# Performance work log

Measured on AMD Instinct MI355X. Metric: run time of the kernel, lower is better.

## Reference

```python
import jax, jax.numpy as jnp
import numpy as np

B, S, D = 8, 1024, 256
H = 8            # num_heads
HD = D // H      # head_dim
FF = 1024        # expert hidden_dim
E = 8            # num_experts
K = 2            # top-k
L = 2            # num_layers
OUT = 1000       # output_dim
EPS = 1e-5


def setup_inputs() -> dict:
    key = jax.random.key(0)
    ks = jax.random.split(key, 20)
    std = 0.02
    inp = {
        "x": jax.random.normal(ks[0], (B, S, D), jnp.float32),
        "qkv_w": jax.random.normal(ks[1], (L, D, 3 * D), jnp.float32) * std,
        "qkv_b": jnp.zeros((L, 3 * D), jnp.float32),
        "attn_w": jax.random.normal(ks[2], (L, D, D), jnp.float32) * std,
        "attn_b": jnp.zeros((L, D), jnp.float32),
        "gate_w": jax.random.normal(ks[3], (L, D, E), jnp.float32) * std,
        "gate_b": jnp.zeros((L, E), jnp.float32),
        "e_w1": jax.random.normal(ks[4], (L, E, D, FF), jnp.float32) * std,
        "e_b1": jnp.zeros((L, E, FF), jnp.float32),
        "e_w2": jax.random.normal(ks[5], (L, E, FF, D), jnp.float32) * std,
        "e_b2": jnp.zeros((L, E, D), jnp.float32),
        "ln1_g": jnp.ones((D,), jnp.float32),
        "ln1_b": jnp.zeros((D,), jnp.float32),
        "ln2_g": jnp.ones((D,), jnp.float32),
        "ln2_b": jnp.zeros((D,), jnp.float32),
        "head_w": jax.random.normal(ks[6], (D, OUT), jnp.float32) * std,
        "head_b": jnp.zeros((OUT,), jnp.float32),
    }
    return inp


def _layer_norm(x, g, b):
    m = jnp.mean(x, -1, keepdims=True)
    v = jnp.mean((x - m) ** 2, -1, keepdims=True)
    return (x - m) / jnp.sqrt(v + EPS) * g + b


def _attention(x, w_qkv, b_qkv, w_o, b_o):
    # x: [B,S,D]
    qkv = (x @ w_qkv + b_qkv).reshape(B, S, 3, H, HD)
    q, k, v = jnp.moveaxis(qkv, 2, 0)            # each [B,S,H,HD]
    q = q.transpose(0, 2, 1, 3)                   # [B,H,S,HD]
    k = k.transpose(0, 2, 1, 3)
    v = v.transpose(0, 2, 1, 3)
    attn = jax.nn.softmax(jnp.einsum('bhqd,bhkd->bhqk', q, k) * (HD ** -0.5), axis=-1)
    o = jnp.einsum('bhqk,bhkd->bhqd', attn, v).transpose(0, 2, 1, 3).reshape(B, S, D)
    return o @ w_o + b_o


def _moe(x, gw, gb, w1, b1, w2, b2):
    # x: [B,S,D] -> tokens [T,D]
    xf = x.reshape(-1, D)
    gates = xf @ gw + gb                           # [T,E]
    scores, idx = jax.lax.top_k(gates, K)          # [T,K]
    gate_w = jax.nn.softmax(scores, axis=-1)       # [T,K]
    # dense all-expert compute, then gather selected experts per token
    h = jax.nn.gelu(jnp.einsum('td,edh->teh', xf, w1) + b1, approximate=False)
    eo = jnp.einsum('teh,ehd->ted', h, w2) + b2    # [T,E,D]
    sel = jnp.take_along_axis(eo, idx[:, :, None], axis=1)  # [T,K,D]
    out = jnp.sum(gate_w[:, :, None] * sel, axis=1)
    return out.reshape(B, S, D)


def reference(x, qkv_w, qkv_b, attn_w, attn_b, gate_w, gate_b,
              e_w1, e_b1, e_w2, e_b2, ln1_g, ln1_b, ln2_g, ln2_b,
              head_w, head_b):
    for l in range(L):
        x = x + _attention(_layer_norm(x, ln1_g, ln1_b),
                           qkv_w[l], qkv_b[l], attn_w[l], attn_b[l])
        x = x + _moe(_layer_norm(x, ln2_g, ln2_b),
                     gate_w[l], gate_b[l], e_w1[l], e_b1[l], e_w2[l], e_b2[l])
    pooled = jnp.mean(x, axis=1)                   # [B,D]
    return pooled @ head_w + head_b                # [B,OUT]
```

## Files before the change

### kernel.cpp

```cpp
#include <hip/hip_runtime.h>
#include <math.h>

#define TOK   8192
#define DIM   256
#define NH    8
#define HDIM  32
#define FFD   1024
#define NE    8
#define NL    2
#define NOUT  1000
#define NSLOT 16384

typedef unsigned int uint;
typedef unsigned short ushort;
typedef __attribute__((ext_vector_type(8))) short short8;
typedef __attribute__((ext_vector_type(4))) float f32x4;

#define WS_X     ((size_t)0)
#define WS_LN    (WS_X    + (size_t)TOK*DIM)
#define WS_QKV   (WS_LN   + (size_t)TOK*DIM)
#define WS_H     (WS_QKV  + (size_t)TOK*3*DIM)
#define WS_SOUT  (WS_H    + (size_t)NSLOT*256)
#define WS_GV    (WS_SOUT + (size_t)NSLOT*256)
#define WS_PP    (WS_GV   + (size_t)TOK*2)
#define WS_POOL  (WS_PP   + (size_t)8*32*256)
#define WS_INT   (WS_POOL + (size_t)8*256)
#define WS_U16   (WS_INT  + (size_t)54144)
#define WS_BIG   (WS_U16  + (size_t)2359296)

#define IB_COUNTS   0
#define IB_NTILES   8
#define IB_OFFS     16
#define IB_CURS     24
#define IB_TILE_E   32
#define IB_TILE_R0  320
#define IB_TILE_RE  608
#define IB_GIDX     896
#define IB_SPOS     17280
#define IB_STOK     33664
#define IB_BLKC     50048
#define IB_BLKB     52096

__device__ __forceinline__ float gelu_exact(float v) {
    return 0.5f * v * (1.0f + erff(v * 0.70710678118654752f));
}

__device__ __forceinline__ ushort rnd_bf16(float x) {
    uint u = __float_as_uint(x);
    return (ushort)((u + 0x7FFFu + ((u >> 16) & 1u)) >> 16);
}

__device__ __forceinline__ float bf16_f32(ushort h) {
    return __uint_as_float(((uint)h) << 16);
}

__device__ __forceinline__ void split2(float x, ushort& h, ushort& lo) {
    uint u = __float_as_uint(x);
    uint hh = (u + 0x7FFFu + ((u >> 16) & 1u)) >> 16;
    h = (ushort)hh;
    float hf = __uint_as_float(hh << 16);
    float l = x - hf;
    uint ul = __float_as_uint(l);
    lo = (ushort)((ul + 0x7FFFu + ((ul >> 16) & 1u)) >> 16);
}

__device__ __forceinline__ void gld16(const ushort* g, ushort* l) {
    __builtin_amdgcn_global_load_lds(
        (const __attribute__((address_space(1))) uint*)g,
        (__attribute__((address_space(3))) uint*)l, 16, 0, 0);
}

template<bool WF32>
__global__ __launch_bounds__(256) void ln_split(const float* __restrict__ x,
                                                float* __restrict__ out,
                                                ushort* __restrict__ ohi,
                                                const float* __restrict__ g,
                                                const float* __restrict__ b) {
    int wave = threadIdx.x >> 6;
    int lane = threadIdx.x & 63;
    int t = blockIdx.x * 4 + wave;
    const float* xp = x + (size_t)t * DIM;
    float4 v = *(const float4*)&xp[lane * 4];
    float s = v.x + v.y + v.z + v.w;
    #pragma unroll
    for (int off = 32; off; off >>= 1) s += __shfl_xor(s, off);
    float mean = s * (1.0f / 256.0f);
    float dx = v.x - mean, dy = v.y - mean, dz = v.z - mean, dw = v.w - mean;
    float vs = dx * dx + dy * dy + dz * dz + dw * dw;
    #pragma unroll
    for (int off = 32; off; off >>= 1) vs += __shfl_xor(vs, off);
    float inv = rsqrtf(vs * (1.0f / 256.0f) + 1e-5f);
    float4 gg = *(const float4*)&g[lane * 4];
    float4 bb = *(const float4*)&b[lane * 4];
    float o0 = dx * inv * gg.x + bb.x;
    float o1 = dy * inv * gg.y + bb.y;
    float o2 = dz * inv * gg.z + bb.z;
    float o3 = dw * inv * gg.w + bb.w;
    size_t idx = (size_t)t * DIM + lane * 4;
    if (WF32) {
        float4 o; o.x = o0; o.y = o1; o.z = o2; o.w = o3;
        *(float4*)&out[idx] = o;
    }
    uint2 ph;
    ph.x = (uint)rnd_bf16(o0) | ((uint)rnd_bf16(o1) << 16);
    ph.y = (uint)rnd_bf16(o2) | ((uint)rnd_bf16(o3) << 16);
    *(uint2*)&ohi[idx] = ph;
}

template<bool WLO>
__global__ __launch_bounds__(256) void split_transpose(const float* __restrict__ src,
                                                       ushort* __restrict__ dhi,
                                                       ushort* __restrict__ dlo,
                                                       int K, int N) {
    int z = blockIdx.z;
    const float* s = src + (size_t)z * K * N;
    ushort* th = dhi + (size_t)z * K * N;
    ushort* tl = dlo + (size_t)z * K * N;
    __shared__ float tile[32][33];
    int k0 = blockIdx.x * 32, n0 = blockIdx.y * 32;
    int tx = threadIdx.x & 31, ty = threadIdx.x >> 5;
    #pragma unroll
    for (int i = 0; i < 4; ++i) {
        int k = k0 + ty + i * 8;
        tile[ty + i * 8][tx] = s[(size_t)k * N + n0 + tx];
    }
    __syncthreads();
    #pragma unroll
    for (int i = 0; i < 4; ++i) {
        int n = n0 + ty + i * 8;
        float v = tile[tx][ty + i * 8];
        ushort h, lo;
        split2(v, h, lo);
        th[(size_t)n * K + k0 + tx] = h;
        if (WLO) tl[(size_t)n * K + k0 + tx] = lo;
    }
}


template<int MODE, int APASS>
__global__ __launch_bounds__(256) void mfma_dense128x64(const ushort* __restrict__ Ah,
                                                        const ushort* __restrict__ Al,
                                                        const ushort* __restrict__ Bh,
                                                        const ushort* __restrict__ Bl,
                                                        const float* __restrict__ bias,
                                                        float* __restrict__ C,
                                                        ushort* __restrict__ Chi, int N) {
    __shared__ ushort LAh[128][32], LBh[64][32], LBl[64][32];
    __shared__ ushort LAl[APASS == 2 ? 128 : 2][32];
    int tid = threadIdx.x;
    int w = tid >> 6, l = tid & 63, c = l & 15, G = l >> 4;
    int row0 = blockIdx.y * 128, col0 = blockIdx.x * 64;
    int lr = l >> 2, sd = l & 3;
    int rA0 = w * 16 + lr, rA1 = 64 + rA0;
    size_t ga0 = (size_t)(row0 + rA0) * 256 + ((sd ^ ((rA0 >> 1) & 3)) << 3);
    size_t ga1 = (size_t)(row0 + rA1) * 256 + ((sd ^ ((rA1 >> 1) & 3)) << 3);
    size_t gb0 = (size_t)(col0 + rA0) * 256 + ((sd ^ ((rA0 >> 1) & 3)) << 3);
    ushort* dA0h = &LAh[w * 16][0];      ushort* dA1h = &LAh[64 + w * 16][0];
    ushort* dBh  = &LBh[w * 16][0];      ushort* dBl  = &LBl[w * 16][0];
    f32x4 acc[2][4] = {};
    for (int k0 = 0; k0 < 256; k0 += 32) {
        gld16(&Ah[ga0 + k0], dA0h);
        gld16(&Ah[ga1 + k0], dA1h);
        if (APASS == 2) {
            gld16(&Al[ga0 + k0], &LAl[w * 16][0]);
            gld16(&Al[ga1 + k0], &LAl[64 + w * 16][0]);
        }
        gld16(&Bh[gb0 + k0], dBh);
        gld16(&Bl[gb0 + k0], dBl);
        __syncthreads();
        int ar = w * 32 + c;
        short8 a_h[2], a_l[2];
        #pragma unroll
        for (int i = 0; i < 2; ++i) {
            int r = ar + i * 16;
            int sg = (G ^ ((r >> 1) & 3)) << 3;
            a_h[i] = *(const short8*)&LAh[r][sg];
            if (APASS == 2) a_l[i] = *(const short8*)&LAl[r][sg];
        }
        #pragma unroll
        for (int j = 0; j < 4; ++j) {
            int r = j * 16 + c;
            int sg = (G ^ ((r >> 1) & 3)) << 3;
            short8 b_h = *(const short8*)&LBh[r][sg];
            short8 b_l = *(const short8*)&LBl[r][sg];
            #pragma unroll
            for (int i = 0; i < 2; ++i) {
                acc[i][j] = __builtin_amdgcn_mfma_f32_16x16x32_bf16(a_h[i], b_h, acc[i][j], 0, 0, 0);
                acc[i][j] = __builtin_amdgcn_mfma_f32_16x16x32_bf16(a_h[i], b_l, acc[i][j], 0, 0, 0);
                if (APASS == 2)
                    acc[i][j] = __builtin_amdgcn_mfma_f32_16x16x32_bf16(a_l[i], b_h, acc[i][j], 0, 0, 0);
            }
        }
        __syncthreads();
    }
    int rbase = row0 + w * 32 + G * 4;
    #pragma unroll
    for (int i = 0; i < 2; ++i) {
        #pragma unroll
        for (int j = 0; j < 4; ++j) {
            int gc = col0 + j * 16 + c;
            float bv = bias[gc];
            #pragma unroll
            for (int rr = 0; rr < 4; ++rr) {
                int grow = rbase + i * 16 + rr;
                size_t idx = (size_t)grow * N + gc;
                float v = acc[i][j][rr] + bv;
                if (MODE == 1) v += C[idx];
                if (MODE == 3) {
                    Chi[idx] = rnd_bf16(v);
                } else {
                    C[idx] = v;
                }
            }
        }
    }
}

__global__ __launch_bounds__(256) void vt_kernel(const ushort* __restrict__ qkvh,
                                                 ushort* __restrict__ vth) {
    int bh = blockIdx.y;
    int b = bh >> 3, h = bh & 7;
    int kv0 = blockIdx.x * 32;
    __shared__ ushort smh[32][33];
    int tid = threadIdx.x;
    #pragma unroll
    for (int p = 0; p < 4; ++p) {
        int kv = p * 8 + (tid >> 5);
        int d = tid & 31;
        size_t src = ((size_t)(b * 1024 + kv0 + kv)) * 768 + 512 + h * 32 + d;
        smh[kv][d] = qkvh[src];
    }
    __syncthreads();
    #pragma unroll
    for (int p = 0; p < 4; ++p) {
        int d = p * 8 + (tid >> 5);
        int kv = tid & 31;
        size_t dst = ((size_t)(bh * 32 + d)) * 1024 + kv0 + kv;
        vth[dst] = smh[kv][d];
    }
}

__global__ __launch_bounds__(256, 4) void attention_mfma(const ushort* __restrict__ qkvh,
                                                         const ushort* __restrict__ vth,
                                                         ushort* __restrict__ ohi) {
    int b = blockIdx.z, h = blockIdx.y;
    int q0 = blockIdx.x * 64;
    int tid = threadIdx.x;
    int w = tid >> 6, l = tid & 63;
    int c = l & 15, g = l >> 4;
    __shared__ ushort Kh[64][40];
    __shared__ ushort VTh[32][72];
    __shared__ ushort Ph[4][16][76];

    size_t qbase = ((size_t)(b * 1024 + q0 + w * 16 + c)) * 768 + h * 32 + g * 8;
    short8 qa_h = *(const short8*)&qkvh[qbase];

    f32x4 acc_o[2] = {};
    float lpart[4] = {0.f, 0.f, 0.f, 0.f};
    const float scale = 0.17677669529663687f;

    int sr = tid >> 2, sc8 = (tid & 3) * 8;
    size_t kgbase = ((size_t)(b * 1024 + sr)) * 768 + 256 + h * 32 + sc8;
    int vd = tid >> 3, vk8 = (tid & 7) * 8;
    size_t vtbase = ((size_t)((b * 8 + h) * 32 + vd)) * 1024 + vk8;

    for (int kv0 = 0; kv0 < 1024; kv0 += 64) {
        __syncthreads();
        *(uint4*)&Kh[sr][sc8]  = *(const uint4*)&qkvh[kgbase + (size_t)kv0 * 768];
        *(uint4*)&VTh[vd][vk8] = *(const uint4*)&vth[vtbase + kv0];
        __syncthreads();

        f32x4 s4[4];
        #pragma unroll
        for (int t = 0; t < 4; ++t) {
            short8 kh = *(const short8*)&Kh[t * 16 + c][g * 8];
            f32x4 a = {};
            a = __builtin_amdgcn_mfma_f32_16x16x32_bf16(qa_h, kh, a, 0, 0, 0);
            s4[t] = a;
        }

        #pragma unroll
        for (int rr = 0; rr < 4; ++rr) {
            float sum = 0.f;
            #pragma unroll
            for (int t = 0; t < 4; ++t) {
                float p = __expf(s4[t][rr] * scale);
                uint u = __float_as_uint(p);
                uint r = (u + 0x7FFFu + ((u >> 16) & 1u)) >> 16;
                Ph[w][g * 4 + rr][t * 16 + c] = (ushort)r;
                sum += __uint_as_float(r << 16);
            }
            lpart[rr] += sum;
        }
        asm volatile("s_waitcnt lgkmcnt(0)" ::: "memory");

        #pragma unroll
        for (int kt = 0; kt < 2; ++kt) {
            short8 pah = *(const short8*)&Ph[w][c][kt * 32 + g * 8];
            #pragma unroll
            for (int T = 0; T < 2; ++T) {
                short8 vh = *(const short8*)&VTh[T * 16 + c][kt * 32 + g * 8];
                acc_o[T] = __builtin_amdgcn_mfma_f32_16x16x32_bf16(pah, vh, acc_o[T], 0, 0, 0);
            }
        }
    }

    #pragma unroll
    for (int rr = 0; rr < 4; ++rr) {
        float s = lpart[rr];
        s += __shfl_xor(s, 1);
        s += __shfl_xor(s, 2);
        s += __shfl_xor(s, 4);
        s += __shfl_xor(s, 8);
        lpart[rr] = s;
    }

    #pragma unroll
    for (int rr = 0; rr < 4; ++rr) {
        float inv = 1.0f / lpart[rr];
        int q = q0 + w * 16 + g * 4 + rr;
        #pragma unroll
        for (int T = 0; T < 2; ++T) {
            float v = acc_o[T][rr] * inv;
            size_t idx = (size_t)(b * 1024 + q) * 256 + h * 32 + T * 16 + c;
            ohi[idx] = rnd_bf16(v);
        }
    }
}

__global__ __launch_bounds__(256) void mfma_ffn1_12864(const ushort* __restrict__ Ah,
                                                       const ushort* __restrict__ W1h,
                                                       const float* __restrict__ b1l,
                                                       ushort* __restrict__ hh,
                                                       const int* __restrict__ ib,
                                                       int c0, int hFF) {
    int tileIdx = blockIdx.y;
    if (tileIdx >= ib[IB_NTILES]) return;
    int e = ib[IB_TILE_E + tileIdx];
    int row0 = ib[IB_TILE_R0 + tileIdx];
    int rowend = ib[IB_TILE_RE + tileIdx];
    __shared__ ushort LAh[128][32], LBh[64][32];
    __shared__ int tok[128];
    int tid = threadIdx.x;
    if (tid < 128) {
        int sr = row0 + tid;
        tok[tid] = ib[IB_STOK + (sr < rowend ? sr : row0)];
    }
    __syncthreads();
    int w = tid >> 6, l = tid & 63, c = l & 15, G = l >> 4;
    int lr = l >> 2, sd = l & 3;
    int rA0 = w * 16 + lr, rA1 = 64 + rA0;
    int colbase = blockIdx.x * 64;
    const ushort* Bh = W1h + (size_t)e * 262144 + (size_t)(c0 + colbase) * 256;
    size_t ga0 = (size_t)tok[rA0] * 256 + ((sd ^ ((rA0 >> 1) & 3)) << 3);
    size_t ga1 = (size_t)tok[rA1] * 256 + ((sd ^ ((rA1 >> 1) & 3)) << 3);
    size_t gb0 = (size_t)rA0 * 256 + ((sd ^ ((rA0 >> 1) & 3)) << 3);
    ushort* dA0h = &LAh[w * 16][0];      ushort* dA1h = &LAh[64 + w * 16][0];
    ushort* dBh  = &LBh[w * 16][0];
    f32x4 acc[2][4] = {};
    for (int k0 = 0; k0 < 256; k0 += 32) {
        gld16(&Ah[ga0 + k0], dA0h);
        gld16(&Ah[ga1 + k0], dA1h);
        gld16(&Bh[gb0 + k0], dBh);
        __syncthreads();
        int ar = w * 32 + c;
        short8 a_h[2];
        #pragma unroll
        for (int i = 0; i < 2; ++i) {
            int r = ar + i * 16;
            int sg = (G ^ ((r >> 1) & 3)) << 3;
            a_h[i] = *(const short8*)&LAh[r][sg];
        }
        #pragma unroll
        for (int j = 0; j < 4; ++j) {
            int r = j * 16 + c;
            int sg = (G ^ ((r >> 1) & 3)) << 3;
            short8 b_h = *(const short8*)&LBh[r][sg];
            #pragma unroll
            for (int i = 0; i < 2; ++i) {
                acc[i][j] = __builtin_amdgcn_mfma_f32_16x16x32_bf16(a_h[i], b_h, acc[i][j], 0, 0, 0);
            }
        }
        __syncthreads();
    }
    int rbase = row0 + w * 32 + G * 4;
    #pragma unroll
    for (int i = 0; i < 2; ++i) {
        #pragma unroll
        for (int j = 0; j < 4; ++j) {
            int cl = colbase + j * 16 + c;
            float bv = b1l[(size_t)e * FFD + c0 + cl];
            #pragma unroll
            for (int rr = 0; rr < 4; ++rr) {
                int sr = rbase + i * 16 + rr;
                if (sr < rowend) {
                    float v = gelu_exact(acc[i][j][rr] + bv);
                    hh[(size_t)sr * hFF + cl] = rnd_bf16(v);
                }
            }
        }
    }
}

template<bool OUT16>
__global__ __launch_bounds__(256) void mfma_ffn2_12864(const ushort* __restrict__ Ah,
                                                       const ushort* __restrict__ W2h,
                                                       const float* __restrict__ b2l,
                                                       float* __restrict__ soutf,
                                                       ushort* __restrict__ soutb,
                                                       const int* __restrict__ ib,
                                                       int c0, int hFF) {
    int tileIdx = blockIdx.y;
    if (tileIdx >= ib[IB_NTILES]) return;
    int e = ib[IB_TILE_E + tileIdx];
    int row0 = ib[IB_TILE_R0 + tileIdx];
    int rowend = ib[IB_TILE_RE + tileIdx];
    __shared__ ushort LAh[128][32], LBh[64][32];
    int tid = threadIdx.x;
    int w = tid >> 6, l = tid & 63, c = l & 15, G = l >> 4;
    int lr = l >> 2, sd = l & 3;
    int rA0 = w * 16 + lr, rA1 = 64 + rA0;
    int colbase = blockIdx.x * 64;
    const ushort* Bh = W2h + (size_t)e * 262144;
    size_t ga0 = (size_t)(row0 + rA0) * hFF + ((sd ^ ((rA0 >> 1) & 3)) << 3);
    size_t ga1 = (size_t)(row0 + rA1) * hFF + ((sd ^ ((rA1 >> 1) & 3)) << 3);
    size_t gb0 = (size_t)(colbase + rA0) * 1024 + c0 + ((sd ^ ((rA0 >> 1) & 3)) << 3);
    ushort* dA0h = &LAh[w * 16][0];      ushort* dA1h = &LAh[64 + w * 16][0];
    ushort* dBh  = &LBh[w * 16][0];
    f32x4 acc[2][4] = {};
    for (int k0 = 0; k0 < hFF; k0 += 32) {
        gld16(&Ah[ga0 + k0], dA0h);
        gld16(&Ah[ga1 + k0], dA1h);
        gld16(&Bh[gb0 + k0], dBh);
        __syncthreads();
        int ar = w * 32 + c;
        short8 a_h[2];
        #pragma unroll
        for (int i = 0; i < 2; ++i) {
            int r = ar + i * 16;
            int sg = (G ^ ((r >> 1) & 3)) << 3;
            a_h[i] = *(const short8*)&LAh[r][sg];
        }
        #pragma unroll
        for (int j = 0; j < 4; ++j) {
            int r = j * 16 + c;
            int sg = (G ^ ((r >> 1) & 3)) << 3;
            short8 b_h = *(const short8*)&LBh[r][sg];
            #pragma unroll
            for (int i = 0; i < 2; ++i) {
                acc[i][j] = __builtin_amdgcn_mfma_f32_16x16x32_bf16(a_h[i], b_h, acc[i][j], 0, 0, 0);
            }
        }
        __syncthreads();
    }
    int rbase = row0 + w * 32 + G * 4;
    #pragma unroll
    for (int i = 0; i < 2; ++i) {
        #pragma unroll
        for (int j = 0; j < 4; ++j) {
            int n = colbase + j * 16 + c;
            float bv = b2l[(size_t)e * DIM + n];
            #pragma unroll
            for (int rr = 0; rr < 4; ++rr) {
                int sr = rbase + i * 16 + rr;
                if (sr < rowend) {
                    size_t idx = (size_t)sr * 256 + n;
                    if (OUT16) {
                        soutb[idx] = rnd_bf16(acc[i][j][rr] + bv);
                    } else {
                        if (c0 == 0) soutf[idx] = acc[i][j][rr] + bv;
                        else         soutf[idx] += acc[i][j][rr];
                    }
                }
            }
        }
    }
}

__global__ __launch_bounds__(256) void gate_topk(const float* __restrict__ lnb,
                                                 const float* __restrict__ gw,
                                                 const float* __restrict__ gb,
                                                 float* __restrict__ gv, int* __restrict__ ib) {
    __shared__ int hist[8];
    int tid = threadIdx.x;
    if (tid < 8) hist[tid] = 0;
    __syncthreads();
    int grp = tid >> 3, ln8 = tid & 7;
    int t = blockIdx.x * 32 + grp;
    const float* x = lnb + (size_t)t * DIM + ln8 * 32;
    const float* wb = gw + (size_t)ln8 * 32 * 8;
    float g[8] = {};
    #pragma unroll
    for (int d4 = 0; d4 < 8; ++d4) {
        float4 xv = *(const float4*)&x[d4 * 4];
        const float* wr = wb + d4 * 32;
        float4 wa0 = *(const float4*)&wr[0],  wb0 = *(const float4*)&wr[4];
        float4 wa1 = *(const float4*)&wr[8],  wb1 = *(const float4*)&wr[12];
        float4 wa2 = *(const float4*)&wr[16], wb2 = *(const float4*)&wr[20];
        float4 wa3 = *(const float4*)&wr[24], wb3 = *(const float4*)&wr[28];
        g[0] += xv.x * wa0.x + xv.y * wa1.x + xv.z * wa2.x + xv.w * wa3.x;
        g[1] += xv.x * wa0.y + xv.y * wa1.y + xv.z * wa2.y + xv.w * wa3.y;
        g[2] += xv.x * wa0.z + xv.y * wa1.z + xv.z * wa2.z + xv.w * wa3.z;
        g[3] += xv.x * wa0.w + xv.y * wa1.w + xv.z * wa2.w + xv.w * wa3.w;
        g[4] += xv.x * wb0.x + xv.y * wb1.x + xv.z * wb2.x + xv.w * wb3.x;
        g[5] += xv.x * wb0.y + xv.y * wb1.y + xv.z * wb2.y + xv.w * wb3.y;
        g[6] += xv.x * wb0.z + xv.y * wb1.z + xv.z * wb2.z + xv.w * wb3.z;
        g[7] += xv.x * wb0.w + xv.y * wb1.w + xv.z * wb2.w + xv.w * wb3.w;
    }
    #pragma unroll
    for (int e = 0; e < 8; ++e) {
        g[e] += __shfl_xor(g[e], 1);
        g[e] += __shfl_xor(g[e], 2);
        g[e] += __shfl_xor(g[e], 4);
    }
    if (ln8 == 0) {
        #pragma unroll
        for (int e = 0; e < 8; ++e) g[e] += gb[e];
        int i0 = 0; float s0 = g[0];
        #pragma unroll
        for (int e = 1; e < 8; ++e) if (g[e] > s0) { s0 = g[e]; i0 = e; }
        int i1 = -1; float s1 = -1e30f;
        #pragma unroll
        for (int e = 0; e < 8; ++e) if (e != i0 && g[e] > s1) { s1 = g[e]; i1 = e; }
        float e1 = __expf(s1 - s0);
        float w0v = 1.0f / (1.0f + e1);
        float w1v = e1 / (1.0f + e1);
        gv[2 * t] = w0v; gv[2 * t + 1] = w1v;
        ib[IB_GIDX + 2 * t] = i0; ib[IB_GIDX + 2 * t + 1] = i1;
        atomicAdd(&hist[i0], 1);
        atomicAdd(&hist[i1], 1);
    }
    __syncthreads();
    if (tid < 8) ib[IB_BLKC + blockIdx.x * 8 + tid] = hist[tid];
}

__global__ __launch_bounds__(256) void scan_tiles(int* ib) {
    __shared__ int bc[2048], bb[2048];
    __shared__ int counts[8], offs[8], tstart[9];
    int tid = threadIdx.x;
    for (int i = tid; i < 2048; i += 256) bc[i] = ib[IB_BLKC + i];
    __syncthreads();
    if (tid < 8) {
        int run = 0;
        for (int b = 0; b < 256; ++b) {
            bb[b * 8 + tid] = run;
            run += bc[b * 8 + tid];
        }
        counts[tid] = run;
    }
    __syncthreads();
    if (tid == 0) {
        int off = 0, ts = 0;
        for (int e = 0; e < 8; ++e) {
            offs[e] = off;
            ib[IB_OFFS + e] = off;
            tstart[e] = ts;
            ib[IB_COUNTS + e] = counts[e];
            ts += (counts[e] + 127) >> 7;
            off += counts[e];
        }
        tstart[8] = ts;
        ib[IB_NTILES] = ts;
    }
    __syncthreads();
    for (int i = tid; i < 2048; i += 256)
        ib[IB_BLKB + i] = offs[i & 7] + bb[i];
    int total = tstart[8];
    for (int idx = tid; idx < total; idx += 256) {
        int e = 0;
        while (idx >= tstart[e + 1]) ++e;
        int i = idx - tstart[e];
        ib[IB_TILE_E + idx] = e;
        ib[IB_TILE_R0 + idx] = offs[e] + i * 128;
        int rem = counts[e] - i * 128;
        ib[IB_TILE_RE + idx] = offs[e] + i * 128 + (rem < 128 ? rem : 128);
    }
}

__global__ __launch_bounds__(64) void scatter_slots(int* ib) {
    __shared__ int cnt8[8];
    int tid = threadIdx.x;
    if (tid < 8) cnt8[tid] = ib[IB_BLKB + blockIdx.x * 8 + tid];
    __syncthreads();
    int t = blockIdx.x * 32 + (tid >> 1);
    int k = tid & 1;
    int e = ib[IB_GIDX + 2 * t + k];
    int pos = atomicAdd(&cnt8[e], 1);
    ib[IB_STOK + pos] = t;
    ib[IB_SPOS + 2 * t + k] = pos;
}

template<bool OUT16>
__global__ __launch_bounds__(64) void moe_gather(float* __restrict__ xb,
                                                 const float* __restrict__ soutf,
                                                 const ushort* __restrict__ soutb,
                                                 const float* __restrict__ gv,
                                                 const int* __restrict__ ib) {
    int t = blockIdx.x;
    int d = threadIdx.x * 4;
    int p0 = ib[IB_SPOS + 2 * t], p1 = ib[IB_SPOS + 2 * t + 1];
    float g0 = gv[2 * t], g1 = gv[2 * t + 1];
    float4 xv = *(float4*)&xb[(size_t)t * 256 + d];
    float s0x, s0y, s0z, s0w, s1x, s1y, s1z, s1w;
    if (OUT16) {
        uint2 a = *(const uint2*)&soutb[(size_t)p0 * 256 + d];
        uint2 bq = *(const uint2*)&soutb[(size_t)p1 * 256 + d];
        s0x = bf16_f32((ushort)(a.x & 0xFFFF));  s0y = bf16_f32((ushort)(a.x >> 16));
        s0z = bf16_f32((ushort)(a.y & 0xFFFF));  s0w = bf16_f32((ushort)(a.y >> 16));
        s1x = bf16_f32((ushort)(bq.x & 0xFFFF)); s1y = bf16_f32((ushort)(bq.x >> 16));
        s1z = bf16_f32((ushort)(bq.y & 0xFFFF)); s1w = bf16_f32((ushort)(bq.y >> 16));
    } else {
        float4 a = *(const float4*)&soutf[(size_t)p0 * 256 + d];
        float4 bq = *(const float4*)&soutf[(size_t)p1 * 256 + d];
        s0x = a.x; s0y = a.y; s0z = a.z; s0w = a.w;
        s1x = bq.x; s1y = bq.y; s1z = bq.z; s1w = bq.w;
    }
    xv.x += g0 * s0x + g1 * s1x;
    xv.y += g0 * s0y + g1 * s1y;
    xv.z += g0 * s0z + g1 * s1z;
    xv.w += g0 * s0w + g1 * s1w;
    *(float4*)&xb[(size_t)t * 256 + d] = xv;
}

__global__ __launch_bounds__(256) void pool1(const float* __restrict__ xb, float* __restrict__ pp) {
    int b = blockIdx.x, ch = blockIdx.y, d = threadIdx.x;
    float s = 0.0f;
    for (int i = 0; i < 32; ++i) s += xb[((size_t)b * 1024 + ch * 32 + i) * 256 + d];
    pp[(size_t)(b * 32 + ch) * 256 + d] = s;
}
__global__ __launch_bounds__(256) void pool2(const float* __restrict__ pp, float* __restrict__ pool) {
    int b = blockIdx.x, d = threadIdx.x;
    float s = 0.0f;
    for (int c = 0; c < 32; ++c) s += pp[(size_t)(b * 32 + c) * 256 + d];
    pool[(size_t)b * 256 + d] = s * (1.0f / 1024.0f);
}

__global__ __launch_bounds__(256) void head_kernel(const float* __restrict__ pool,
                                                   const float* __restrict__ hw,
                                                   const float* __restrict__ hb,
                                                   float* __restrict__ out) {
    __shared__ float P[2048];
    int tid = threadIdx.x;
    for (int i = tid; i < 2048; i += 256) P[i] = pool[i];
    __syncthreads();
    int j = blockIdx.x * 256 + tid;
    if (j >= NOUT) return;
    float acc[8] = {};
    for (int d = 0; d < 256; ++d) {
        float w = hw[(size_t)d * NOUT + j];
        #pragma unroll
        for (int b = 0; b < 8; ++b) acc[b] += P[b * 256 + d] * w;
    }
    #pragma unroll
    for (int b = 0; b < 8; ++b) out[(size_t)b * NOUT + j] = acc[b] + hb[j];
}

extern "C" void kernel_launch(void* const* d_in, const int* in_sizes, int n_in,
                              void* d_out, int out_size, void* d_ws, size_t ws_size,
                              hipStream_t stream) {
    const float* x      = (const float*)d_in[0];
    const float* qkv_w  = (const float*)d_in[1];
    const float* qkv_b  = (const float*)d_in[2];
    const float* attn_w = (const float*)d_in[3];
    const float* attn_b = (const float*)d_in[4];
    const float* gate_w = (const float*)d_in[5];
    const float* gate_b = (const float*)d_in[6];
    const float* e_w1   = (const float*)d_in[7];
    const float* e_b1   = (const float*)d_in[8];
    const float* e_w2   = (const float*)d_in[9];
    const float* e_b2   = (const float*)d_in[10];
    const float* ln1_g  = (const float*)d_in[11];
    const float* ln1_b  = (const float*)d_in[12];
    const float* ln2_g  = (const float*)d_in[13];
    const float* ln2_b  = (const float*)d_in[14];
    const float* head_w = (const float*)d_in[15];
    const float* head_b = (const float*)d_in[16];
    float* out = (float*)d_out;
    float* wsf = (float*)d_ws;

    float* xb   = wsf + WS_X;
    float* lnb  = wsf + WS_LN;
    float* sobf = wsf + WS_SOUT;
    ushort* sobb = (ushort*)(wsf + WS_SOUT);
    float* gv   = wsf + WS_GV;
    float* pp   = wsf + WS_PP;
    float* pool = wsf + WS_POOL;
    int*   ib   = (int*)(wsf + WS_INT);

    ushort* qkvsh = (ushort*)(wsf + WS_QKV);
    ushort* wT    = (ushort*)(wsf + WS_QKV);
    ushort* w1th  = wT;
    ushort* w2th  = wT + 4194304;
    ushort* wTdummy = wT + 6291456;

    ushort* vth = (ushort*)(wsf + WS_H);

    ushort* u16  = (ushort*)(wsf + WS_U16);
    ushort* lnh  = u16;
    ushort* qwh  = u16 + 4194304;
    ushort* qwl  = u16 + 4390912;
    ushort* awh  = u16 + 4587520;
    ushort* awl  = u16 + 4653056;

    size_t base_bytes = (size_t)WS_BIG * 4;
    int hFF = 256;
    if (ws_size >= base_bytes + (size_t)NSLOT * 1024 * 2)      hFF = 1024;
    else if (ws_size >= base_bytes + (size_t)NSLOT * 512 * 2)  hFF = 512;
    ushort* hh = (hFF == 256) ? (ushort*)(wsf + WS_H) : (ushort*)(wsf + WS_BIG);
    int NCC = 1024 / hFF;

    hipMemcpyAsync(xb, x, (size_t)TOK * DIM * sizeof(float), hipMemcpyDeviceToDevice, stream);

    for (int l = 0; l < NL; ++l) {
        ln_split<false><<<TOK / 4, 256, 0, stream>>>(xb, nullptr, lnh, ln1_g, ln1_b);
        split_transpose<true><<<dim3(8, 24, 1), 256, 0, stream>>>(
            qkv_w + (size_t)l * DIM * 3 * DIM, qwh, qwl, 256, 768);
        mfma_dense128x64<3, 1><<<dim3(12, 64), 256, 0, stream>>>(
            lnh, nullptr, qwh, qwl, qkv_b + (size_t)l * 3 * DIM, nullptr, qkvsh, 768);
        vt_kernel<<<dim3(32, 64), 256, 0, stream>>>(qkvsh, vth);
        attention_mfma<<<dim3(16, NH, 8), 256, 0, stream>>>(qkvsh, vth, lnh);
        split_transpose<true><<<dim3(8, 8, 1), 256, 0, stream>>>(
            attn_w + (size_t)l * DIM * DIM, awh, awl, 256, 256);
        mfma_dense128x64<1, 1><<<dim3(4, 64), 256, 0, stream>>>(
            lnh, nullptr, awh, awl, attn_b + (size_t)l * DIM, xb, nullptr, 256);

        ln_split<true><<<TOK / 4, 256, 0, stream>>>(xb, lnb, lnh, ln2_g, ln2_b);
        split_transpose<false><<<dim3(8, 32, 8), 256, 0, stream>>>(
            e_w1 + (size_t)l * NE * DIM * FFD, w1th, wTdummy, 256, 1024);
        split_transpose<false><<<dim3(32, 8, 8), 256, 0, stream>>>(
            e_w2 + (size_t)l * NE * FFD * DIM, w2th, wTdummy, 1024, 256);
        gate_topk<<<TOK / 32, 256, 0, stream>>>(
            lnb, gate_w + (size_t)l * DIM * NE, gate_b + (size_t)l * NE, gv, ib);
        scan_tiles<<<1, 256, 0, stream>>>(ib);
        scatter_slots<<<TOK / 32, 64, 0, stream>>>(ib);
        if (NCC == 1) {
            mfma_ffn1_12864<<<dim3(16, 136), 256, 0, stream>>>(
                lnh, w1th, e_b1 + (size_t)l * NE * FFD, hh, ib, 0, 1024);
            mfma_ffn2_12864<true><<<dim3(4, 136), 256, 0, stream>>>(
                hh, w2th, e_b2 + (size_t)l * NE * DIM, nullptr, sobb, ib, 0, 1024);
            moe_gather<true><<<TOK, 64, 0, stream>>>(xb, nullptr, sobb, gv, ib);
        } else {
            for (int c = 0; c < NCC; ++c) {
                mfma_ffn1_12864<<<dim3(hFF / 64, 136), 256, 0, stream>>>(
                    lnh, w1th, e_b1 + (size_t)l * NE * FFD, hh, ib, c * hFF, hFF);
                mfma_ffn2_12864<false><<<dim3(4, 136), 256, 0, stream>>>(
                    hh, w2th, e_b2 + (size_t)l * NE * DIM, sobf, nullptr, ib, c * hFF, hFF);
            }
            moe_gather<false><<<TOK, 64, 0, stream>>>(xb, sobf, nullptr, gv, ib);
        }
    }

    pool1<<<dim3(8, 32), 256, 0, stream>>>(xb, pp);
    pool2<<<8, 256, 0, stream>>>(pp, pool);
    head_kernel<<<4, 256, 0, stream>>>(pool, head_w, head_b, out);
}
```

Measured before the change: 371.3 us.

## Merge weight transposes, fold V transpose into attention, fuse pooling into head

Merges the qkv and attention-output weight split/transpose launches into one kernel, and the two expert weight transposes into another. Drops the separate V-transpose kernel: attention now loads V rows directly and scatters them transposed into shared memory. Folds the second pooling stage into the head kernel. The aim is to cut kernel-launch count and an intermediate global round trip. The cost is scalar, possibly bank-conflicted shared-memory stores in the attention loop, and redundant pooling work in each head block.

```diff
diff --git a/kernel.cpp b/kernel.cpp
--- a/kernel.cpp
+++ b/kernel.cpp
@@ -107,17 +107,11 @@
     *(uint2*)&ohi[idx] = ph;
 }
 
-template<bool WLO>
-__global__ __launch_bounds__(256) void split_transpose(const float* __restrict__ src,
-                                                       ushort* __restrict__ dhi,
-                                                       ushort* __restrict__ dlo,
-                                                       int K, int N) {
-    int z = blockIdx.z;
-    const float* s = src + (size_t)z * K * N;
-    ushort* th = dhi + (size_t)z * K * N;
-    ushort* tl = dlo + (size_t)z * K * N;
+__device__ __forceinline__ void st_body(const float* __restrict__ s,
+                                        ushort* __restrict__ th,
+                                        ushort* __restrict__ tl,
+                                        int K, int N, int k0, int n0, bool wlo) {
     __shared__ float tile[32][33];
-    int k0 = blockIdx.x * 32, n0 = blockIdx.y * 32;
     int tx = threadIdx.x & 31, ty = threadIdx.x >> 5;
     #pragma unroll
     for (int i = 0; i < 4; ++i) {
@@ -132,7 +126,35 @@
         ushort h, lo;
         split2(v, h, lo);
         th[(size_t)n * K + k0 + tx] = h;
-        if (WLO) tl[(size_t)n * K + k0 + tx] = lo;
+        if (wlo) tl[(size_t)n * K + k0 + tx] = lo;
+    }
+}
+
+__global__ __launch_bounds__(256) void st_attn_weights(const float* __restrict__ qkvw,
+                                                       const float* __restrict__ attnw,
+                                                       ushort* __restrict__ qwh,
+                                                       ushort* __restrict__ qwl,
+                                                       ushort* __restrict__ awh,
+                                                       ushort* __restrict__ awl) {
+    int y = blockIdx.y;
+    int k0 = blockIdx.x * 32;
+    if (y < 24) st_body(qkvw, qwh, qwl, 256, 768, k0, y * 32, true);
+    else        st_body(attnw, awh, awl, 256, 256, k0, (y - 24) * 32, true);
+}
+
+__global__ __launch_bounds__(256) void st_expert_weights(const float* __restrict__ w1,
+                                                         const float* __restrict__ w2,
+                                                         ushort* __restrict__ w1th,
+                                                         ushort* __restrict__ w2th) {
+    int z = blockIdx.y;
+    int idx = blockIdx.x;
+    if (idx < 256) {
+        int k0 = (idx & 7) * 32, n0 = (idx >> 3) * 32;
+        st_body(w1 + (size_t)z * 262144, w1th + (size_t)z * 262144, nullptr, 256, 1024, k0, n0, false);
+    } else {
+        idx -= 256;
+        int k0 = (idx & 31) * 32, n0 = (idx >> 5) * 32;
+        st_body(w2 + (size_t)z * 262144, w2th + (size_t)z * 262144, nullptr, 1024, 256, k0, n0, false);
     }
 }
 
@@ -216,32 +238,7 @@
     }
 }
 
-__global__ __launch_bounds__(256) void vt_kernel(const ushort* __restrict__ qkvh,
-                                                 ushort* __restrict__ vth) {
-    int bh = blockIdx.y;
-    int b = bh >> 3, h = bh & 7;
-    int kv0 = blockIdx.x * 32;
-    __shared__ ushort smh[32][33];
-    int tid = threadIdx.x;
-    #pragma unroll
-    for (int p = 0; p < 4; ++p) {
-        int kv = p * 8 + (tid >> 5);
-        int d = tid & 31;
-        size_t src = ((size_t)(b * 1024 + kv0 + kv)) * 768 + 512 + h * 32 + d;
-        smh[kv][d] = qkvh[src];
-    }
-    __syncthreads();
-    #pragma unroll
-    for (int p = 0; p < 4; ++p) {
-        int d = p * 8 + (tid >> 5);
-        int kv = tid & 31;
-        size_t dst = ((size_t)(bh * 32 + d)) * 1024 + kv0 + kv;
-        vth[dst] = smh[kv][d];
-    }
-}
-
 __global__ __launch_bounds__(256, 4) void attention_mfma(const ushort* __restrict__ qkvh,
-                                                         const ushort* __restrict__ vth,
                                                          ushort* __restrict__ ohi) {
     int b = blockIdx.z, h = blockIdx.y;
     int q0 = blockIdx.x * 64;
@@ -261,13 +258,16 @@
 
     int sr = tid >> 2, sc8 = (tid & 3) * 8;
     size_t kgbase = ((size_t)(b * 1024 + sr)) * 768 + 256 + h * 32 + sc8;
-    int vd = tid >> 3, vk8 = (tid & 7) * 8;
-    size_t vtbase = ((size_t)((b * 8 + h) * 32 + vd)) * 1024 + vk8;
+    int vkv = tid >> 2, vd8 = (tid & 3) * 8;
+    size_t vgbase = ((size_t)(b * 1024 + vkv)) * 768 + 512 + h * 32 + vd8;
 
     for (int kv0 = 0; kv0 < 1024; kv0 += 64) {
         __syncthreads();
-        *(uint4*)&Kh[sr][sc8]  = *(const uint4*)&qkvh[kgbase + (size_t)kv0 * 768];
-        *(uint4*)&VTh[vd][vk8] = *(const uint4*)&vth[vtbase + kv0];
+        *(uint4*)&Kh[sr][sc8] = *(const uint4*)&qkvh[kgbase + (size_t)kv0 * 768];
+        uint4 vv = *(const uint4*)&qkvh[vgbase + (size_t)kv0 * 768];
+        const ushort* vsc = (const ushort*)&vv;
+        #pragma unroll
+        for (int j = 0; j < 8; ++j) VTh[vd8 + j][vkv] = vsc[j];
         __syncthreads();
 
         f32x4 s4[4];
@@ -628,20 +628,20 @@
     for (int i = 0; i < 32; ++i) s += xb[((size_t)b * 1024 + ch * 32 + i) * 256 + d];
     pp[(size_t)(b * 32 + ch) * 256 + d] = s;
 }
-__global__ __launch_bounds__(256) void pool2(const float* __restrict__ pp, float* __restrict__ pool) {
-    int b = blockIdx.x, d = threadIdx.x;
-    float s = 0.0f;
-    for (int c = 0; c < 32; ++c) s += pp[(size_t)(b * 32 + c) * 256 + d];
-    pool[(size_t)b * 256 + d] = s * (1.0f / 1024.0f);
-}
-
-__global__ __launch_bounds__(256) void head_kernel(const float* __restrict__ pool,
+
+__global__ __launch_bounds__(256) void head_kernel(const float* __restrict__ pp,
                                                    const float* __restrict__ hw,
                                                    const float* __restrict__ hb,
                                                    float* __restrict__ out) {
     __shared__ float P[2048];
     int tid = threadIdx.x;
-    for (int i = tid; i < 2048; i += 256) P[i] = pool[i];
+    for (int i = tid; i < 2048; i += 256) {
+        int b = i >> 8, d = i & 255;
+        float s = 0.0f;
+        #pragma unroll 8
+        for (int c = 0; c < 32; ++c) s += pp[(size_t)(b * 32 + c) * 256 + d];
+        P[i] = s * (1.0f / 1024.0f);
+    }
     __syncthreads();
     int j = blockIdx.x * 256 + tid;
     if (j >= NOUT) return;
@@ -684,16 +684,12 @@
     ushort* sobb = (ushort*)(wsf + WS_SOUT);
     float* gv   = wsf + WS_GV;
     float* pp   = wsf + WS_PP;
-    float* pool = wsf + WS_POOL;
     int*   ib   = (int*)(wsf + WS_INT);
 
     ushort* qkvsh = (ushort*)(wsf + WS_QKV);
     ushort* wT    = (ushort*)(wsf + WS_QKV);
     ushort* w1th  = wT;
     ushort* w2th  = wT + 4194304;
-    ushort* wTdummy = wT + 6291456;
-
-    ushort* vth = (ushort*)(wsf + WS_H);
 
     ushort* u16  = (ushort*)(wsf + WS_U16);
     ushort* lnh  = u16;
@@ -713,22 +709,18 @@
 
     for (int l = 0; l < NL; ++l) {
         ln_split<false><<<TOK / 4, 256, 0, stream>>>(xb, nullptr, lnh, ln1_g, ln1_b);
-        split_transpose<true><<<dim3(8, 24, 1), 256, 0, stream>>>(
-            qkv_w + (size_t)l * DIM * 3 * DIM, qwh, qwl, 256, 768);
+        st_attn_weights<<<dim3(8, 32), 256, 0, stream>>>(
+            qkv_w + (size_t)l * DIM * 3 * DIM, attn_w + (size_t)l * DIM * DIM,
+            qwh, qwl, awh, awl);
         mfma_dense128x64<3, 1><<<dim3(12, 64), 256, 0, stream>>>(
             lnh, nullptr, qwh, qwl, qkv_b + (size_t)l * 3 * DIM, nullptr, qkvsh, 768);
-        vt_kernel<<<dim3(32, 64), 256, 0, stream>>>(qkvsh, vth);
-        attention_mfma<<<dim3(16, NH, 8), 256, 0, stream>>>(qkvsh, vth, lnh);
-        split_transpose<true><<<dim3(8, 8, 1), 256, 0, stream>>>(
-            attn_w + (size_t)l * DIM * DIM, awh, awl, 256, 256);
+        attention_mfma<<<dim3(16, NH, 8), 256, 0, stream>>>(qkvsh, lnh);
         mfma_dense128x64<1, 1><<<dim3(4, 64), 256, 0, stream>>>(
             lnh, nullptr, awh, awl, attn_b + (size_t)l * DIM, xb, nullptr, 256);
 
         ln_split<true><<<TOK / 4, 256, 0, stream>>>(xb, lnb, lnh, ln2_g, ln2_b);
-        split_transpose<false><<<dim3(8, 32, 8), 256, 0, stream>>>(
-            e_w1 + (size_t)l * NE * DIM * FFD, w1th, wTdummy, 256, 1024);
-        split_transpose<false><<<dim3(32, 8, 8), 256, 0, stream>>>(
-            e_w2 + (size_t)l * NE * FFD * DIM, w2th, wTdummy, 1024, 256);
+        st_expert_weights<<<dim3(512, 8), 256, 0, stream>>>(
+            e_w1 + (size_t)l * NE * DIM * FFD, e_w2 + (size_t)l * NE * FFD * DIM, w1th, w2th);
         gate_topk<<<TOK / 32, 256, 0, stream>>>(
             lnb, gate_w + (size_t)l * DIM * NE, gate_b + (size_t)l * NE, gv, ib);
         scan_tiles<<<1, 256, 0, stream>>>(ib);
@@ -751,6 +743,5 @@
     }
 
     pool1<<<dim3(8, 32), 256, 0, stream>>>(xb, pp);
-    pool2<<<8, 256, 0, stream>>>(pp, pool);
-    head_kernel<<<4, 256, 0, stream>>>(pool, head_w, head_b, out);
-}
+    head_kernel<<<4, 256, 0, stream>>>(pp, head_w, head_b, out);
+}
```

Result: no change. 374.8 us (+0.9%).
